# Kernel optimization log

Measured on AMD Instinct MI355X. Metric: run time of the kernel, lower is better.

Reference implementation:

```python
import jax, jax.numpy as jnp
import numpy as np

E = 1024      # h_dim
H = 16        # num_heads
D = E // H    # head_dim = 64
O = 1024      # o_dim == q_dim
EPS = 1e-5


def _rotate_half(x):
    d = x.shape[-1]
    x1, x2 = x[..., : d // 2], x[..., d // 2 :]
    return jnp.concatenate([-x2, x1], axis=-1)


def setup_inputs() -> dict:
    key = jax.random.key(0)
    ks = jax.random.split(key, 12)
    B, S = 8, 1024
    s = 0.02
    return {
        "query": jax.random.normal(ks[0], (B, S, O), jnp.float32),
        "key": jax.random.normal(ks[1], (B, S, O), jnp.float32),
        "value": jax.random.normal(ks[2], (B, S, O), jnp.float32),
        "Wq": jax.random.normal(ks[3], (E, O), jnp.float32) * s,
        "Wk": jax.random.normal(ks[4], (E, O), jnp.float32) * s,
        "Wv": jax.random.normal(ks[5], (E, O), jnp.float32) * s,
        "in_proj_w": jax.random.normal(ks[6], (3 * E, E), jnp.float32) * s,
        "out_proj_w": jax.random.normal(ks[7], (E, E), jnp.float32) * s,
        "proj_w": jax.random.normal(ks[8], (O, E), jnp.float32) * s,
        "gamma": jnp.ones((O,), jnp.float32),
        "beta": jnp.zeros((O,), jnp.float32),
    }


def reference(query, key, value, Wq, Wk, Wv, in_proj_w, out_proj_w, proj_w, gamma, beta):
    B, S, _ = query.shape
    # [B,S,*] -> [S,B,*] then bias-free linears
    q = jnp.swapaxes(query, 0, 1) @ Wq.T  # [S,B,E]
    k = jnp.swapaxes(key, 0, 1) @ Wk.T
    v = jnp.swapaxes(value, 0, 1) @ Wv.T

    # RoPE (faithful quirk: positions indexed along the BATCH axis B)
    inv_freq = 1.0 / (10000.0 ** (jnp.arange(0, D, 2, dtype=jnp.float32) / D))
    t = jnp.arange(B, dtype=jnp.float32)
    freqs = t[:, None] * inv_freq[None, :]            # [B, D/2]
    emb = jnp.concatenate([freqs, freqs], axis=-1)    # [B, D]
    cos = jnp.cos(emb)[None, :, None, :]              # [1,B,1,D]
    sin = jnp.sin(emb)[None, :, None, :]

    q4 = q.reshape(S, B, H, D)
    k4 = k.reshape(S, B, H, D)
    q_emb = (q4 * cos + _rotate_half(q4) * sin).reshape(S, B, E)
    k_emb = (k4 * cos + _rotate_half(k4) * sin).reshape(S, B, E)

    # nn.MultiheadAttention (bias=False, batch_first=False)
    Wqa, Wka, Wva = in_proj_w[:E], in_proj_w[E : 2 * E], in_proj_w[2 * E :]
    qp = (q_emb @ Wqa.T).reshape(S, B, H, D)
    kp = (k_emb @ Wka.T).reshape(S, B, H, D)
    vp = (v @ Wva.T).reshape(S, B, H, D)

    scale = 1.0 / np.sqrt(D).astype(np.float32)
    scores = jnp.einsum("sbhd,tbhd->bhst", qp, kp) * scale  # [B,H,S,S]
    attn = jax.nn.softmax(scores, axis=-1)
    o = jnp.einsum("bhst,tbhd->sbhd", attn, vp).reshape(S, B, E)
    o = o @ out_proj_w.T                                     # [S,B,E]

    # output proj + residual + LayerNorm
    ob = jnp.swapaxes(o, 0, 1) @ proj_w.T                    # [B,S,O]
    x = query + ob
    mu = jnp.mean(x, axis=-1, keepdims=True)
    var = jnp.mean((x - mu) ** 2, axis=-1, keepdims=True)
    return (x - mu) * jax.lax.rsqrt(var + EPS) * gamma + beta
```

## Files before the change

kernel.cpp:

```cpp
#include <hip/hip_runtime.h>
#include <hip/hip_bf16.h>
#include <stdint.h>

typedef __bf16 bf16;
typedef __attribute__((ext_vector_type(8))) __bf16 bf16x8;
typedef __attribute__((ext_vector_type(4))) float f32x4;

#define NEG_LN10K_32 (-0.28782313662425575f)

__device__ __forceinline__ bf16x8 cvt8(f32x4 a, f32x4 b) {
    bf16x8 r;
    r[0] = (bf16)a[0]; r[1] = (bf16)a[1]; r[2] = (bf16)a[2]; r[3] = (bf16)a[3];
    r[4] = (bf16)b[0]; r[5] = (bf16)b[1]; r[6] = (bf16)b[2]; r[7] = (bf16)b[3];
    return r;
}

__device__ __forceinline__ void async_copy16(bf16* lds, const bf16* g) {
    __builtin_amdgcn_global_load_lds((const __attribute__((address_space(1))) void*)g,
                                     (__attribute__((address_space(3))) void*)lds, 16, 0, 0);
}

__global__ __launch_bounds__(256) void wconv6(
    const float* __restrict__ s0, const float* __restrict__ s1, const float* __restrict__ s2,
    const float* __restrict__ s3, const float* __restrict__ s4, const float* __restrict__ s5,
    bf16* __restrict__ d0, bf16* __restrict__ d1, bf16* __restrict__ d2,
    bf16* __restrict__ d3, bf16* __restrict__ d4, bf16* __restrict__ d5)
{
    const int z = blockIdx.z;
    const float* src; bf16* dst;
    switch (z) {
        case 0: src = s0; dst = d0; break;
        case 1: src = s1; dst = d1; break;
        case 2: src = s2; dst = d2; break;
        case 3: src = s3; dst = d3; break;
        case 4: src = s4; dst = d4; break;
        default: src = s5; dst = d5; break;
    }
    const size_t i = ((size_t)blockIdx.x * 256 + threadIdx.x) * 8;
    *(bf16x8*)(dst + i) = cvt8(*(const f32x4*)(src + i), *(const f32x4*)(src + i + 4));
}

__global__ __launch_bounds__(256) void prepT(
    const float* __restrict__ in0, const float* __restrict__ in1,
    bf16* __restrict__ out0, bf16* __restrict__ out1)
{
    const float* in = blockIdx.z ? in1 : in0;
    bf16* out       = blockIdx.z ? out1 : out0;
    __shared__ float tile[64 * 65];
    const int t  = threadIdx.x;
    const int i0 = blockIdx.y * 64, j0 = blockIdx.x * 64;
    const int r  = t >> 2, cg = (t & 3) * 16;
#pragma unroll
    for (int c = 0; c < 16; c += 4) {
        const f32x4 v = *(const f32x4*)(in + (size_t)(i0 + r) * 1024 + j0 + cg + c);
        tile[r * 65 + cg + c + 0] = v[0];
        tile[r * 65 + cg + c + 1] = v[1];
        tile[r * 65 + cg + c + 2] = v[2];
        tile[r * 65 + cg + c + 3] = v[3];
    }
    __syncthreads();
    bf16x8 o0v, o1v;
#pragma unroll
    for (int ii = 0; ii < 8; ++ii) {
        o0v[ii] = (bf16)tile[(cg + ii) * 65 + r];
        o1v[ii] = (bf16)tile[(cg + 8 + ii) * 65 + r];
    }
    bf16* dst = out + (size_t)(j0 + r) * 1024 + i0 + cg;
    *(bf16x8*)dst       = o0v;
    *(bf16x8*)(dst + 8) = o1v;
}

template<int AF32, int WF32>
__global__ __launch_bounds__(256) void gemm_bt(
    const void* __restrict__ A0v, const void* __restrict__ A1v, const void* __restrict__ A2v,
    const void* __restrict__ W0v, const void* __restrict__ W1v, const void* __restrict__ W2v,
    bf16* __restrict__ C0, bf16* __restrict__ C1, bf16* __restrict__ C2,
    const float* __restrict__ R0, int rope_mask)
{
    const int z = blockIdx.z;
    const void* Av = (z == 0) ? A0v : ((z == 1) ? A1v : A2v);
    const void* Wp = (z == 0) ? W0v : ((z == 1) ? W1v : W2v);
    bf16*       C  = (z == 0) ? C0 : ((z == 1) ? C1 : C2);
    const float* R = (z == 0) ? R0 : nullptr;
    const bool doRope = ((rope_mask >> z) & 1) != 0;

    __shared__ __attribute__((aligned(16))) bf16 sA[2][128 * 32];
    __shared__ __attribute__((aligned(16))) bf16 sB[2][128 * 32];

    const int t    = threadIdx.x;
    const int w    = t >> 6;
    const int lane = t & 63;
    const int l16  = lane & 15;
    const int quad = lane >> 4;
    const int wrow = w >> 1;
    const int wcol = w & 1;

    int m0, n0;
    if (gridDim.y == 64) {
        const int fs   = blockIdx.y * 8 + blockIdx.x;
        const int xcd  = fs & 7;
        const int slot = fs >> 3;
        m0 = ((xcd << 3) | (slot >> 3)) * 128;
        n0 = (slot & 7) * 128;
    } else {
        m0 = blockIdx.y * 128;
        n0 = blockIdx.x * 128;
    }

    const int sgr = ((t & 3) ^ ((t >> 3) & 3)) * 8;
    const size_t aOff = (size_t)(m0 + (t >> 2)) * 1024 + sgr;
    const size_t wOff = (size_t)(n0 + (t >> 2)) * 1024 + sgr;
    const int qs = (quad ^ ((l16 >> 1) & 3)) * 8;

    f32x4 arg[4], brg[4];

    auto loadAreg = [&](int k0) {
        const float* g = (const float*)Av;
        arg[0] = *(const f32x4*)(g + aOff + k0);
        arg[1] = *(const f32x4*)(g + aOff + k0 + 4);
        arg[2] = *(const f32x4*)(g + aOff + 65536 + k0);
        arg[3] = *(const f32x4*)(g + aOff + 65536 + k0 + 4);
    };
    auto loadBreg = [&](int k0) {
        const float* g = (const float*)Wp;
        brg[0] = *(const f32x4*)(g + wOff + k0);
        brg[1] = *(const f32x4*)(g + wOff + k0 + 4);
        brg[2] = *(const f32x4*)(g + wOff + 65536 + k0);
        brg[3] = *(const f32x4*)(g + wOff + 65536 + k0 + 4);
    };
    auto writeAreg = [&](int b) {
        *(bf16x8*)&sA[b][t * 8]        = cvt8(arg[0], arg[1]);
        *(bf16x8*)&sA[b][t * 8 + 2048] = cvt8(arg[2], arg[3]);
    };
    auto writeBreg = [&](int b) {
        *(bf16x8*)&sB[b][t * 8]        = cvt8(brg[0], brg[1]);
        *(bf16x8*)&sB[b][t * 8 + 2048] = cvt8(brg[2], brg[3]);
    };
    auto stageAasync = [&](int k0, int b) {
        const bf16* g = (const bf16*)Av;
        async_copy16(&sA[b][w * 512],        g + aOff + k0);
        async_copy16(&sA[b][w * 512 + 2048], g + aOff + 65536 + k0);
    };
    auto stageBasync = [&](int k0, int b) {
        const bf16* g = (const bf16*)Wp;
        async_copy16(&sB[b][w * 512],        g + wOff + k0);
        async_copy16(&sB[b][w * 512 + 2048], g + wOff + 65536 + k0);
    };

    f32x4 acc[4][4];
#pragma unroll
    for (int i = 0; i < 4; ++i)
#pragma unroll
        for (int j = 0; j < 4; ++j)
            acc[i][j] = (f32x4){0.f, 0.f, 0.f, 0.f};

    if constexpr (AF32) loadAreg(0);
    if constexpr (WF32) loadBreg(0);
    if constexpr (!AF32) stageAasync(0, 0);
    if constexpr (!WF32) stageBasync(0, 0);
    if constexpr (AF32 && WF32)      asm volatile("s_waitcnt vmcnt(0)" ::: "memory");
    else if constexpr (AF32 || WF32) asm volatile("s_waitcnt vmcnt(2)" ::: "memory");
    if constexpr (AF32) writeAreg(0);
    if constexpr (WF32) writeBreg(0);
    if constexpr (AF32) loadAreg(32);
    if constexpr (WF32) loadBreg(32);
    if constexpr (!AF32 && !WF32)    asm volatile("s_waitcnt vmcnt(0) lgkmcnt(0)\ns_barrier" ::: "memory");
    else if constexpr (AF32 && WF32) asm volatile("s_waitcnt lgkmcnt(0)\ns_barrier" ::: "memory");
    else                             asm volatile("s_waitcnt vmcnt(4) lgkmcnt(0)\ns_barrier" ::: "memory");

    for (int k0 = 0; k0 < 1024; k0 += 32) {
        const int buf = (k0 >> 5) & 1;
        const int nb  = buf ^ 1;
        const int nxt = k0 + 32;

        if (nxt < 1024) {
            if constexpr (!AF32) stageAasync(nxt, nb);
            if constexpr (!WF32) stageBasync(nxt, nb);
        }

        bf16x8 af[4], bw[4];
#pragma unroll
        for (int mi = 0; mi < 4; ++mi)
            af[mi] = *(const bf16x8*)&sA[buf][(wrow * 64 + mi * 16 + l16) * 32 + qs];
#pragma unroll
        for (int ni = 0; ni < 4; ++ni)
            bw[ni] = *(const bf16x8*)&sB[buf][(wcol * 64 + ni * 16 + l16) * 32 + qs];
#pragma unroll
        for (int mi = 0; mi < 4; ++mi)
#pragma unroll
            for (int ni = 0; ni < 4; ++ni)
                acc[mi][ni] = __builtin_amdgcn_mfma_f32_16x16x32_bf16(af[mi], bw[ni], acc[mi][ni], 0, 0, 0);

        if constexpr (AF32 || WF32) {
            if (nxt < 1024) {
                if constexpr (AF32 && WF32) asm volatile("s_waitcnt vmcnt(0)" ::: "memory");
                else                        asm volatile("s_waitcnt vmcnt(2)" ::: "memory");
                if constexpr (AF32) writeAreg(nb);
                if constexpr (WF32) writeBreg(nb);
                if (k0 + 64 < 1024) {
                    if constexpr (AF32) loadAreg(k0 + 64);
                    if constexpr (WF32) loadBreg(k0 + 64);
                }
            }
        }

        if (nxt < 1024) {
            if constexpr (!AF32 && !WF32)
                asm volatile("s_waitcnt vmcnt(0) lgkmcnt(0)\ns_barrier" ::: "memory");
            else if constexpr (AF32 && WF32)
                asm volatile("s_waitcnt lgkmcnt(0)\ns_barrier" ::: "memory");
            else {
                if (k0 + 64 < 1024) asm volatile("s_waitcnt vmcnt(4) lgkmcnt(0)\ns_barrier" ::: "memory");
                else                asm volatile("s_waitcnt vmcnt(0) lgkmcnt(0)\ns_barrier" ::: "memory");
            }
        }
    }

    if (doRope) {
        const float bb = (float)(m0 >> 10);
        float s0, c0v, s1, c1v;
        sincosf(bb * expf((float)l16 * NEG_LN10K_32), &s0, &c0v);
        sincosf(bb * expf((float)(16 + l16) * NEG_LN10K_32), &s1, &c1v);
#pragma unroll
        for (int mi = 0; mi < 4; ++mi) {
#pragma unroll
            for (int r = 0; r < 4; ++r) {
                float x1 = acc[mi][0][r], x2 = acc[mi][2][r];
                acc[mi][0][r] = x1 * c0v - x2 * s0;
                acc[mi][2][r] = x2 * c0v + x1 * s0;
                x1 = acc[mi][1][r]; x2 = acc[mi][3][r];
                acc[mi][1][r] = x1 * c1v - x2 * s1;
                acc[mi][3][r] = x2 * c1v + x1 * s1;
            }
        }
    }

#pragma unroll
    for (int mi = 0; mi < 4; ++mi) {
#pragma unroll
        for (int ni = 0; ni < 4; ++ni) {
            const int col = n0 + wcol * 64 + ni * 16 + l16;
#pragma unroll
            for (int r = 0; r < 4; ++r) {
                const int row = m0 + wrow * 64 + mi * 16 + quad * 4 + r;
                float v = acc[mi][ni][r];
                if (R) v += R[(size_t)row * 1024 + col];
                C[(size_t)row * 1024 + col] = (bf16)v;
            }
        }
    }
}

__global__ __launch_bounds__(256) void attn_kernel(
    bf16* __restrict__ QP, const bf16* __restrict__ KP, const bf16* __restrict__ VP)
{
    const int fs   = blockIdx.y * 8 + blockIdx.x;
    const int xcd  = fs & 7;
    const int slot = fs >> 3;
    const int qt   = slot & 7;
    const int bh   = (xcd << 4) | (slot >> 3);
    const int tb = (bh >> 4) << 10;
    const int fb = (bh & 15) << 6;

    __shared__ __attribute__((aligned(16))) bf16 sK0[64 * 32];
    __shared__ __attribute__((aligned(16))) bf16 sK1[64 * 32];
    __shared__ __attribute__((aligned(16))) bf16 sVt[64 * 72];
    __shared__ __attribute__((aligned(16))) bf16 sP[4][32 * 72];

    const int t    = threadIdx.x;
    const int w    = t >> 6;
    const int lane = t & 63;
    const int l16  = lane & 15;
    const int quad = lane >> 4;

    const int sgr = ((t & 3) ^ ((t >> 3) & 3)) * 8;
    const int qs  = (quad ^ ((l16 >> 1) & 3)) * 8;

    bf16x8 qf[2][2];
#pragma unroll
    for (int mi = 0; mi < 2; ++mi)
#pragma unroll
        for (int kd = 0; kd < 2; ++kd)
            qf[mi][kd] = *(const bf16x8*)&QP[(size_t)(tb + qt * 128 + w * 32 + mi * 16 + l16) * 1024
                                            + fb + kd * 32 + quad * 8];

    f32x4 oacc[2][4];
#pragma unroll
    for (int i = 0; i < 2; ++i)
#pragma unroll
        for (int j = 0; j < 4; ++j)
            oacc[i][j] = (f32x4){0.f, 0.f, 0.f, 0.f};
    float psum[2][4];
#pragma unroll
    for (int i = 0; i < 2; ++i)
#pragma unroll
        for (int r = 0; r < 4; ++r) psum[i][r] = 0.f;

    auto ldK = [&](int kt, bf16x8& a, bf16x8& b) {
        const bf16* kRow = KP + (size_t)(tb + kt * 64 + (t >> 2)) * 1024 + fb + sgr;
        a = *(const bf16x8*)(kRow);
        b = *(const bf16x8*)(kRow + 32);
    };
    auto ldV = [&](int kt, bf16x8& a, bf16x8& b) {
        const bf16* vRow = VP + (size_t)(tb + kt * 64 + lane) * 1024 + fb;
        a = *(const bf16x8*)(vRow + w * 8);
        b = *(const bf16x8*)(vRow + (w + 4) * 8);
    };

    bf16x8 vk0, vk1, vv0, vv1;
    ldK(0, vk0, vk1);
    ldV(0, vv0, vv1);

    for (int kt = 0; kt < 16; ++kt) {
        __syncthreads();
        *(bf16x8*)&sK0[t * 8] = vk0;
        *(bf16x8*)&sK1[t * 8] = vk1;
#pragma unroll
        for (int j = 0; j < 8; ++j) sVt[(w * 8 + j) * 72 + lane]       = vv0[j];
#pragma unroll
        for (int j = 0; j < 8; ++j) sVt[((w + 4) * 8 + j) * 72 + lane] = vv1[j];

        bf16x8 nk0, nk1, nv0, nv1;
        const bool more = (kt + 1 < 16);
        if (more) {
            ldK(kt + 1, nk0, nk1);
            ldV(kt + 1, nv0, nv1);
        }
        __syncthreads();

        bf16x8 kf[4][2];
#pragma unroll
        for (int ni = 0; ni < 4; ++ni) {
            kf[ni][0] = *(const bf16x8*)&sK0[(ni * 16 + l16) * 32 + qs];
            kf[ni][1] = *(const bf16x8*)&sK1[(ni * 16 + l16) * 32 + qs];
        }
        f32x4 sfr[2][4];
#pragma unroll
        for (int mi = 0; mi < 2; ++mi)
#pragma unroll
            for (int ni = 0; ni < 4; ++ni) {
                f32x4 a = (f32x4){0.f, 0.f, 0.f, 0.f};
                a = __builtin_amdgcn_mfma_f32_16x16x32_bf16(qf[mi][0], kf[ni][0], a, 0, 0, 0);
                a = __builtin_amdgcn_mfma_f32_16x16x32_bf16(qf[mi][1], kf[ni][1], a, 0, 0, 0);
                sfr[mi][ni] = a * 0.125f;
            }

#pragma unroll
        for (int mi = 0; mi < 2; ++mi)
#pragma unroll
            for (int ni = 0; ni < 4; ++ni)
#pragma unroll
                for (int r = 0; r < 4; ++r) {
                    const float p = __expf(sfr[mi][ni][r]);
                    sfr[mi][ni][r] = p;
                    psum[mi][r] += p;
                }

        bf16* sPw = &sP[w][0];
#pragma unroll
        for (int mi = 0; mi < 2; ++mi)
#pragma unroll
            for (int ni = 0; ni < 4; ++ni)
#pragma unroll
                for (int r = 0; r < 4; ++r)
                    sPw[(mi * 16 + quad * 4 + r) * 72 + ni * 16 + l16] = (bf16)sfr[mi][ni][r];
        asm volatile("s_waitcnt lgkmcnt(0)" ::: "memory");

#pragma unroll
        for (int kd = 0; kd < 2; ++kd) {
            bf16x8 pf[2], vf[4];
#pragma unroll
            for (int mi = 0; mi < 2; ++mi)
                pf[mi] = *(const bf16x8*)&sPw[(mi * 16 + l16) * 72 + kd * 32 + quad * 8];
#pragma unroll
            for (int di = 0; di < 4; ++di)
                vf[di] = *(const bf16x8*)&sVt[(di * 16 + l16) * 72 + kd * 32 + quad * 8];
#pragma unroll
            for (int mi = 0; mi < 2; ++mi)
#pragma unroll
                for (int di = 0; di < 4; ++di)
                    oacc[mi][di] = __builtin_amdgcn_mfma_f32_16x16x32_bf16(pf[mi], vf[di], oacc[mi][di], 0, 0, 0);
        }

        if (more) { vk0 = nk0; vk1 = nk1; vv0 = nv0; vv1 = nv1; }
    }

#pragma unroll
    for (int mi = 0; mi < 2; ++mi) {
#pragma unroll
        for (int r = 0; r < 4; ++r) {
            float l = psum[mi][r];
            l += __shfl_xor(l, 1);
            l += __shfl_xor(l, 2);
            l += __shfl_xor(l, 4);
            l += __shfl_xor(l, 8);
            const float inv = 1.f / l;
            const int row = tb + qt * 128 + w * 32 + mi * 16 + quad * 4 + r;
#pragma unroll
            for (int di = 0; di < 4; ++di) {
                const int col = fb + di * 16 + l16;
                QP[(size_t)row * 1024 + col] = (bf16)(oacc[mi][di][r] * inv);
            }
        }
    }
}

__global__ __launch_bounds__(128) void ln_kernel(const bf16* __restrict__ X,
                                                 const float* __restrict__ G,
                                                 const float* __restrict__ Bt,
                                                 float* __restrict__ Y)
{
    const int row = blockIdx.x;
    const int t   = threadIdx.x;
    const size_t base = (size_t)row * 1024 + t * 8;
    const bf16x8 xv = *(const bf16x8*)(X + base);
    float f[8];
    float s = 0.f, s2 = 0.f;
#pragma unroll
    for (int j = 0; j < 8; ++j) { f[j] = (float)xv[j]; s += f[j]; s2 += f[j] * f[j]; }
#pragma unroll
    for (int off = 1; off < 64; off <<= 1) { s += __shfl_xor(s, off); s2 += __shfl_xor(s2, off); }
    __shared__ float ss[2], ssq[2];
    if ((t & 63) == 0) { ss[t >> 6] = s; ssq[t >> 6] = s2; }
    __syncthreads();
    s  = ss[0] + ss[1];
    s2 = ssq[0] + ssq[1];
    const float mu  = s * (1.f / 1024.f);
    const float inv = rsqrtf(s2 * (1.f / 1024.f) - mu * mu + 1e-5f);
    const f32x4 g0 = *(const f32x4*)(G + t * 8);
    const f32x4 g1 = *(const f32x4*)(G + t * 8 + 4);
    const f32x4 b0 = *(const f32x4*)(Bt + t * 8);
    const f32x4 b1 = *(const f32x4*)(Bt + t * 8 + 4);
    f32x4 y0, y1;
#pragma unroll
    for (int j = 0; j < 4; ++j) {
        y0[j] = (f[j]     - mu) * inv * g0[j] + b0[j];
        y1[j] = (f[j + 4] - mu) * inv * g1[j] + b1[j];
    }
    *(f32x4*)(Y + base)     = y0;
    *(f32x4*)(Y + base + 4) = y1;
}

extern "C" void kernel_launch(void* const* d_in, const int* in_sizes, int n_in,
                              void* d_out, int out_size, void* d_ws, size_t ws_size,
                              hipStream_t stream)
{
    const float* query = (const float*)d_in[0];
    const float* key   = (const float*)d_in[1];
    const float* value = (const float*)d_in[2];
    const float* Wq    = (const float*)d_in[3];
    const float* Wk    = (const float*)d_in[4];
    const float* Wv    = (const float*)d_in[5];
    const float* ipw   = (const float*)d_in[6];
    const float* opw   = (const float*)d_in[7];
    const float* pw    = (const float*)d_in[8];
    const float* gamma = (const float*)d_in[9];
    const float* beta  = (const float*)d_in[10];

    const size_t ACT = (size_t)8192 * 1024;
    const size_t MW  = 1048576;
    bf16* o0 = (bf16*)d_out;
    bf16* o1 = o0 + ACT;

    dim3 blk(256);
    dim3 g3(8, 64, 3);
    dim3 g1(8, 64, 1);
    dim3 ga(8, 128);

    const bool full = ws_size >= (6 * MW + 2 * ACT) * sizeof(bf16);

    if (full) {
        bf16* wq  = (bf16*)d_ws;
        bf16* wk  = wq + MW;
        bf16* wqa = wq + 2 * MW;
        bf16* wka = wq + 3 * MW;
        bf16* Fv  = wq + 4 * MW;
        bf16* Fo  = wq + 5 * MW;
        bf16* sltA = wq + 6 * MW;
        bf16* sltB = sltA + ACT;
        bf16* tWva = sltA;
        bf16* tpw  = sltA + MW;
        bf16* WvT  = sltB;
        bf16* opwT = sltB + MW;

        wconv6<<<dim3(512, 1, 6), blk, 0, stream>>>(
            Wq, Wk, ipw, ipw + MW, ipw + 2 * MW, pw,
            wq, wk, wqa, wka, tWva, tpw);
        prepT<<<dim3(16, 16, 2), blk, 0, stream>>>(Wv, opw, WvT, opwT);
        gemm_bt<0, 0><<<dim3(8, 8, 2), blk, 0, stream>>>(
            tWva, tpw, tpw, WvT, opwT, opwT, Fv, Fo, Fo, nullptr, 0);
        gemm_bt<1, 0><<<g3, blk, 0, stream>>>(query, key, value, wq, wk, Fv,
                                              sltA, sltB, o0, nullptr, 0b011);
        gemm_bt<0, 0><<<g1, blk, 0, stream>>>(sltA, sltA, sltA, wqa, wqa, wqa,
                                              o1, o1, o1, nullptr, 0);
        gemm_bt<0, 0><<<g1, blk, 0, stream>>>(sltB, sltB, sltB, wka, wka, wka,
                                              sltA, sltA, sltA, nullptr, 0);
        attn_kernel<<<ga, blk, 0, stream>>>(o1, sltA, o0);
        gemm_bt<0, 0><<<g1, blk, 0, stream>>>(o1, o1, o1, Fo, Fo, Fo,
                                              sltB, sltB, sltB, query, 0);
        ln_kernel<<<8192, 128, 0, stream>>>(sltB, gamma, beta, (float*)d_out);
    } else {
        bf16* b0 = (bf16*)d_ws;
        bf16* b1 = b0 + ACT;
        gemm_bt<1, 1><<<g3, blk, 0, stream>>>(query, key, value, Wq, Wk, Wv,
                                              b0, b1, o0, nullptr, 0b011);
        gemm_bt<0, 1><<<g1, blk, 0, stream>>>(o0, o0, o0, ipw + 2 * MW, ipw, ipw,
                                              o1, o1, o1, nullptr, 0);
        gemm_bt<0, 1><<<g1, blk, 0, stream>>>(b0, b0, b0, ipw, ipw, ipw,
                                              o0, o0, o0, nullptr, 0);
        gemm_bt<0, 1><<<g1, blk, 0, stream>>>(b1, b1, b1, ipw + MW, ipw, ipw,
                                              b0, b0, b0, nullptr, 0);
        attn_kernel<<<ga, blk, 0, stream>>>(o0, b0, o1);
        gemm_bt<0, 1><<<g1, blk, 0, stream>>>(o0, o0, o0, opw, opw, opw,
                                              b0, b0, b0, nullptr, 0);
        gemm_bt<0, 1><<<g1, blk, 0, stream>>>(b0, b0, b0, pw, pw, pw,
                                              b1, b1, b1, query, 0);
        ln_kernel<<<8192, 128, 0, stream>>>(b1, gamma, beta, (float*)d_out);
    }
}
```

Before: 493.0 us.

## Load GEMM weight fragments directly from global memory, dropping B LDS staging

The GEMM kernel no longer stages the weight (B) tile through shared memory. Each wave now loads its bf16x8 (or fp32-converted) B fragments straight from global memory every k-step, and only A stays double-buffered in LDS. The software pipeline is simplified to a single prefetch of A with a barrier per iteration, and the attention kernel's __syncthreads are replaced by explicit lgkmcnt waits plus s_barrier. This removes LDS traffic and capacity for B, which may raise occupancy, but it relies on L1/L2 reuse for B across waves and exposes global-load latency inside the MFMA loop without prefetching.

Result: slower. 549.4 us (+11.4%).

```diff
diff --git a/kernel.cpp b/kernel.cpp
--- a/kernel.cpp
+++ b/kernel.cpp
@@ -7,6 +7,9 @@
 typedef __attribute__((ext_vector_type(4))) float f32x4;
 
 #define NEG_LN10K_32 (-0.28782313662425575f)
+
+#define BAR_LGKM()   { asm volatile("s_waitcnt lgkmcnt(0)" ::: "memory"); __builtin_amdgcn_s_barrier(); }
+#define BAR_VMLGKM() { asm volatile("s_waitcnt vmcnt(0) lgkmcnt(0)" ::: "memory"); __builtin_amdgcn_s_barrier(); }
 
 __device__ __forceinline__ bf16x8 cvt8(f32x4 a, f32x4 b) {
     bf16x8 r;
@@ -85,7 +88,6 @@
     const bool doRope = ((rope_mask >> z) & 1) != 0;
 
     __shared__ __attribute__((aligned(16))) bf16 sA[2][128 * 32];
-    __shared__ __attribute__((aligned(16))) bf16 sB[2][128 * 32];
 
     const int t    = threadIdx.x;
     const int w    = t >> 6;
@@ -109,10 +111,11 @@
 
     const int sgr = ((t & 3) ^ ((t >> 3) & 3)) * 8;
     const size_t aOff = (size_t)(m0 + (t >> 2)) * 1024 + sgr;
-    const size_t wOff = (size_t)(n0 + (t >> 2)) * 1024 + sgr;
     const int qs = (quad ^ ((l16 >> 1) & 3)) * 8;
 
-    f32x4 arg[4], brg[4];
+    const size_t bBase = (size_t)(n0 + wcol * 64 + l16) * 1024 + quad * 8;
+
+    f32x4 arg[4];
 
     auto loadAreg = [&](int k0) {
         const float* g = (const float*)Av;
@@ -121,31 +124,15 @@
         arg[2] = *(const f32x4*)(g + aOff + 65536 + k0);
         arg[3] = *(const f32x4*)(g + aOff + 65536 + k0 + 4);
     };
-    auto loadBreg = [&](int k0) {
-        const float* g = (const float*)Wp;
-        brg[0] = *(const f32x4*)(g + wOff + k0);
-        brg[1] = *(const f32x4*)(g + wOff + k0 + 4);
-        brg[2] = *(const f32x4*)(g + wOff + 65536 + k0);
-        brg[3] = *(const f32x4*)(g + wOff + 65536 + k0 + 4);
-    };
     auto writeAreg = [&](int b) {
         *(bf16x8*)&sA[b][t * 8]        = cvt8(arg[0], arg[1]);
         *(bf16x8*)&sA[b][t * 8 + 2048] = cvt8(arg[2], arg[3]);
-    };
-    auto writeBreg = [&](int b) {
-        *(bf16x8*)&sB[b][t * 8]        = cvt8(brg[0], brg[1]);
-        *(bf16x8*)&sB[b][t * 8 + 2048] = cvt8(brg[2], brg[3]);
     };
     auto stageAasync = [&](int k0, int b) {
         const bf16* g = (const bf16*)Av;
         async_copy16(&sA[b][w * 512],        g + aOff + k0);
         async_copy16(&sA[b][w * 512 + 2048], g + aOff + 65536 + k0);
     };
-    auto stageBasync = [&](int k0, int b) {
-        const bf16* g = (const bf16*)Wp;
-        async_copy16(&sB[b][w * 512],        g + wOff + k0);
-        async_copy16(&sB[b][w * 512 + 2048], g + wOff + 65536 + k0);
-    };
 
     f32x4 acc[4][4];
 #pragma unroll
@@ -154,66 +141,50 @@
         for (int j = 0; j < 4; ++j)
             acc[i][j] = (f32x4){0.f, 0.f, 0.f, 0.f};
 
-    if constexpr (AF32) loadAreg(0);
-    if constexpr (WF32) loadBreg(0);
-    if constexpr (!AF32) stageAasync(0, 0);
-    if constexpr (!WF32) stageBasync(0, 0);
-    if constexpr (AF32 && WF32)      asm volatile("s_waitcnt vmcnt(0)" ::: "memory");
-    else if constexpr (AF32 || WF32) asm volatile("s_waitcnt vmcnt(2)" ::: "memory");
-    if constexpr (AF32) writeAreg(0);
-    if constexpr (WF32) writeBreg(0);
-    if constexpr (AF32) loadAreg(32);
-    if constexpr (WF32) loadBreg(32);
-    if constexpr (!AF32 && !WF32)    asm volatile("s_waitcnt vmcnt(0) lgkmcnt(0)\ns_barrier" ::: "memory");
-    else if constexpr (AF32 && WF32) asm volatile("s_waitcnt lgkmcnt(0)\ns_barrier" ::: "memory");
-    else                             asm volatile("s_waitcnt vmcnt(4) lgkmcnt(0)\ns_barrier" ::: "memory");
+    if constexpr (AF32) {
+        loadAreg(0);
+        writeAreg(0);
+        BAR_LGKM();
+    } else {
+        stageAasync(0, 0);
+        BAR_VMLGKM();
+    }
 
     for (int k0 = 0; k0 < 1024; k0 += 32) {
         const int buf = (k0 >> 5) & 1;
         const int nb  = buf ^ 1;
-        const int nxt = k0 + 32;
-
-        if (nxt < 1024) {
-            if constexpr (!AF32) stageAasync(nxt, nb);
-            if constexpr (!WF32) stageBasync(nxt, nb);
-        }
-
-        bf16x8 af[4], bw[4];
-#pragma unroll
-        for (int mi = 0; mi < 4; ++mi)
-            af[mi] = *(const bf16x8*)&sA[buf][(wrow * 64 + mi * 16 + l16) * 32 + qs];
-#pragma unroll
-        for (int ni = 0; ni < 4; ++ni)
-            bw[ni] = *(const bf16x8*)&sB[buf][(wcol * 64 + ni * 16 + l16) * 32 + qs];
-#pragma unroll
-        for (int mi = 0; mi < 4; ++mi)
+        const bool more = (k0 + 32 < 1024);
+
+        if (more) {
+            if constexpr (AF32) loadAreg(k0 + 32);
+            else                stageAasync(k0 + 32, nb);
+        }
+
+        bf16x8 bw[4];
+#pragma unroll
+        for (int ni = 0; ni < 4; ++ni) {
+            if constexpr (WF32) {
+                const float* p = (const float*)Wp + bBase + ni * 16384 + k0;
+                bw[ni] = cvt8(*(const f32x4*)p, *(const f32x4*)(p + 4));
+            } else {
+                bw[ni] = *(const bf16x8*)((const bf16*)Wp + bBase + ni * 16384 + k0);
+            }
+        }
+
+#pragma unroll
+        for (int mi = 0; mi < 4; ++mi) {
+            const bf16x8 af = *(const bf16x8*)&sA[buf][(wrow * 64 + mi * 16 + l16) * 32 + qs];
 #pragma unroll
             for (int ni = 0; ni < 4; ++ni)
-                acc[mi][ni] = __builtin_amdgcn_mfma_f32_16x16x32_bf16(af[mi], bw[ni], acc[mi][ni], 0, 0, 0);
-
-        if constexpr (AF32 || WF32) {
-            if (nxt < 1024) {
-                if constexpr (AF32 && WF32) asm volatile("s_waitcnt vmcnt(0)" ::: "memory");
-                else                        asm volatile("s_waitcnt vmcnt(2)" ::: "memory");
-                if constexpr (AF32) writeAreg(nb);
-                if constexpr (WF32) writeBreg(nb);
-                if (k0 + 64 < 1024) {
-                    if constexpr (AF32) loadAreg(k0 + 64);
-                    if constexpr (WF32) loadBreg(k0 + 64);
-                }
-            }
-        }
-
-        if (nxt < 1024) {
-            if constexpr (!AF32 && !WF32)
-                asm volatile("s_waitcnt vmcnt(0) lgkmcnt(0)\ns_barrier" ::: "memory");
-            else if constexpr (AF32 && WF32)
-                asm volatile("s_waitcnt lgkmcnt(0)\ns_barrier" ::: "memory");
-            else {
-                if (k0 + 64 < 1024) asm volatile("s_waitcnt vmcnt(4) lgkmcnt(0)\ns_barrier" ::: "memory");
-                else                asm volatile("s_waitcnt vmcnt(0) lgkmcnt(0)\ns_barrier" ::: "memory");
-            }
-        }
+                acc[mi][ni] = __builtin_amdgcn_mfma_f32_16x16x32_bf16(af, bw[ni], acc[mi][ni], 0, 0, 0);
+        }
+
+        if (more) {
+            if constexpr (AF32) writeAreg(nb);
+        }
+
+        if constexpr (AF32) { BAR_LGKM(); }
+        else                { BAR_VMLGKM(); }
     }
 
     if (doRope) {
@@ -312,7 +283,7 @@
     ldV(0, vv0, vv1);
 
     for (int kt = 0; kt < 16; ++kt) {
-        __syncthreads();
+        BAR_LGKM();
         *(bf16x8*)&sK0[t * 8] = vk0;
         *(bf16x8*)&sK1[t * 8] = vk1;
 #pragma unroll
@@ -326,7 +297,7 @@
             ldK(kt + 1, nk0, nk1);
             ldV(kt + 1, nv0, nv1);
         }
-        __syncthreads();
+        BAR_LGKM();
 
         bf16x8 kf[4][2];
 #pragma unroll
```
